# Kernel tuning notes

Hardware: AMD Instinct MI355X
Metric: run time of the kernel (lower is better)

Reference implementation:

```python
import jax, jax.numpy as jnp
import numpy as np

IN_DIM = 768
D_MODEL = 256
B, T = 64, 2048
LN_EPS = 1e-5


def setup_inputs() -> dict:
    key = jax.random.key(0)
    ks = jax.random.split(key, 8)
    s_in = 1.0 / np.sqrt(IN_DIM)
    s_d = 1.0 / np.sqrt(D_MODEL)
    return {
        "x": jax.random.normal(ks[0], (B, T, IN_DIM), dtype=jnp.float32),
        "ln_gamma": jnp.ones((IN_DIM,), jnp.float32),
        "ln_beta": jnp.zeros((IN_DIM,), jnp.float32),
        "W_proj": jax.random.uniform(ks[1], (IN_DIM, D_MODEL), jnp.float32, -s_in, s_in),
        "b_proj": jax.random.uniform(ks[2], (D_MODEL,), jnp.float32, -s_in, s_in),
        "W1": jax.random.uniform(ks[3], (D_MODEL, D_MODEL), jnp.float32, -s_d, s_d),
        "b1": jax.random.uniform(ks[4], (D_MODEL,), jnp.float32, -s_d, s_d),
        "W2": jax.random.uniform(ks[5], (D_MODEL,), jnp.float32, -s_d, s_d),
        "b2": jax.random.uniform(ks[6], (), jnp.float32, -s_d, s_d),
    }


def reference(x, ln_gamma, ln_beta, W_proj, b_proj, W1, b1, W2, b2):
    # nan/inf sanitization to 0
    x = jnp.nan_to_num(x, nan=0.0, posinf=0.0, neginf=0.0)
    # LayerNorm over last dim (biased variance, eps=1e-5)
    mu = jnp.mean(x, axis=-1, keepdims=True)
    var = jnp.mean(jnp.square(x - mu), axis=-1, keepdims=True)
    xn = (x - mu) * jax.lax.rsqrt(var + LN_EPS) * ln_gamma + ln_beta
    # projection to d_model: [B, T, D]
    h = jnp.einsum('btf,fd->btd', xn, W_proj) + b_proj
    # tanh-MLP attention scores: [B, T]
    a = jnp.tanh(jnp.einsum('btd,de->bte', h, W1) + b1)
    w = jnp.einsum('bte,e->bt', a, W2) + b2
    w = jax.nn.softmax(w, axis=-1)
    # weighted-sum pooling over T: [B, D]
    return jnp.einsum('btd,bt->bd', h, w)
```

## Files before the change

kernel.cpp:

```cpp
#include <hip/hip_runtime.h>

#define LN_EPS 1e-5f

typedef __attribute__((ext_vector_type(8))) short s8vec;
typedef __attribute__((ext_vector_type(4))) float f4vec;

#define OFF_WPT   0u
#define OFF_W1F   393216u
#define OFF_U     524288u
#define OFF_C     525312u
#define OFF_UPART 526336u
#define OFF_VPART 575488u
#define OFF_PM    624640u
#define OFF_PS    632832u
#define OFF_PO    641024u

#define BAR()     asm volatile("s_barrier" ::: "memory")
#define WAIT_V4() asm volatile("s_waitcnt vmcnt(4) lgkmcnt(0)" ::: "memory")
#define WAIT_V0() asm volatile("s_waitcnt vmcnt(0) lgkmcnt(0)" ::: "memory")
#define WAIT_L0() asm volatile("s_waitcnt lgkmcnt(0)" ::: "memory")
#define ORDER_FENCE() do { asm volatile("" ::: "memory"); \
                           __builtin_amdgcn_sched_barrier(0); } while (0)

__device__ __forceinline__ unsigned short f2bf(float f) {
  unsigned int u = __float_as_uint(f);
  u += 0x7fffu + ((u >> 16) & 1u);
  return (unsigned short)(u >> 16);
}
__device__ __forceinline__ float bf2f(unsigned short h) {
  return __uint_as_float(((unsigned int)h) << 16);
}
__device__ __forceinline__ void gll16(const void* g, void* l) {
  __builtin_amdgcn_global_load_lds(
      (const __attribute__((address_space(1))) unsigned int*)g,
      (__attribute__((address_space(3))) unsigned int*)l, 16, 0, 0);
}

__global__ void k0_prep(const float* __restrict__ Wp,
                        const float* __restrict__ gamma,
                        const float* __restrict__ beta,
                        const float* __restrict__ W1,
                        char* __restrict__ ws) {
  const int blk = blockIdx.x;
  const int n = threadIdx.x;
  if (blk < 48) {
    unsigned short* wpt = (unsigned short*)(ws + OFF_WPT);
    const int sw = (n & 7) << 4;
    const int k0 = blk * 16;
    float up = 0.f, vp = 0.f;
#pragma unroll
    for (int j = 0; j < 16; ++j) {
      const int k = k0 + j;
      const float w = Wp[k * 256 + n];
      const float wpv = gamma[k] * w;
      up += wpv;
      vp += beta[k] * w;
      const int c = k >> 6, kc = k & 63;
      wpt[c * 16384 + n * 64 + ((((kc * 2) ^ sw)) >> 1)] = f2bf(wpv);
    }
    ((float*)(ws + OFF_UPART))[blk * 256 + n] = up;
    ((float*)(ws + OFF_VPART))[blk * 256 + n] = vp;
  } else {
    unsigned short* w1f = (unsigned short*)(ws + OFF_W1F);
    const int d0 = (blk - 48) * 16;
    const int t = n >> 4, lre = n & 15;
#pragma unroll
    for (int jj = 0; jj < 16; ++jj) {
      const int d = d0 + jj;
      const int ks = d >> 5, lqd = (d >> 3) & 3, j = d & 7;
      w1f[(((t * 8 + ks) * 64) + lqd * 16 + lre) * 8 + j] = f2bf(W1[d * 256 + n]);
    }
  }
}

__global__ void k0_reduce(const float* __restrict__ bproj, char* __restrict__ ws) {
  const int n = threadIdx.x;
  const float* upart = (const float*)(ws + OFF_UPART);
  const float* vpart = (const float*)(ws + OFF_VPART);
  float u = 0.f, v = 0.f;
  for (int i = 0; i < 48; ++i) {
    u += upart[i * 256 + n];
    v += vpart[i * 256 + n];
  }
  ((float*)(ws + OFF_U))[n] = u;
  ((float*)(ws + OFF_C))[n] = v + bproj[n];
}

__global__ __launch_bounds__(256, 2)
void k1_main(const float* __restrict__ x,
             const float* __restrict__ b1,
             const float* __restrict__ W2,
             char* __restrict__ ws) {
  __shared__ __align__(16) char sm[40960];
  char* const sm_a = sm;
  char* const sm_b = sm + 8192;
  char* const sm_h = sm + 8192;
  float* const f_b1 = (float*)sm;
  float* const f_w2 = (float*)(sm + 1024);
  float* const f_lp = (float*)(sm + 2048);
  float* const f_lg = (float*)(sm + 3072);
  float* const f_e  = (float*)(sm + 3328);
  float* const f_mu = (float*)(sm + 3584);
  float* const f_iv = (float*)(sm + 3840);

  const int tid  = threadIdx.x;
  const int lane = tid & 63;
  const int wid  = tid >> 6;
  const int lr = lane & 15;
  const int lq = lane >> 4;

  const int arow = tid >> 2;
  const int aq   = tid & 3;
  const float* xrow = x + (size_t)(blockIdx.x * 64 + arow) * 768 + aq * 16;

  const char* bsrc = (const char*)ws + OFF_WPT + wid * 8192 + lane * 16;
  char*       bdst = sm_b + wid * 8192 + lane * 16;

  const f4vec fz = {0.f, 0.f, 0.f, 0.f};
  f4vec acc[4][4];
#pragma unroll
  for (int m = 0; m < 4; ++m)
#pragma unroll
    for (int n = 0; n < 4; ++n) acc[m][n] = fz;

  float s1 = 0.f, s2 = 0.f;
  float4 vaA[4], vaB[4];
#pragma unroll
  for (int j = 0; j < 4; ++j) vaA[j] = *(const float4*)(xrow + 0 * 64 + j * 4);
#pragma unroll
  for (int j = 0; j < 4; ++j) vaB[j] = *(const float4*)(xrow + 1 * 64 + j * 4);

  auto p1body = [&](int c, float4 (&va)[4], bool pf) {
#pragma unroll
    for (int s = 0; s < 8; ++s) gll16(bsrc + c * 32768 + s * 1024, bdst + s * 1024);
    ORDER_FENCE();
    float v[16];
#pragma unroll
    for (int j = 0; j < 4; ++j) {
      v[4*j+0] = va[j].x; v[4*j+1] = va[j].y; v[4*j+2] = va[j].z; v[4*j+3] = va[j].w;
    }
    unsigned int pk[8];
#pragma unroll
    for (int j = 0; j < 16; ++j) {
      float f = v[j];
      if ((__float_as_uint(f) & 0x7f800000u) == 0x7f800000u) f = 0.f;
      s1 += f; s2 += f * f;
      const unsigned int hb = f2bf(f);
      if ((j & 1) == 0) pk[j >> 1] = hb; else pk[j >> 1] |= hb << 16;
    }
    {
      const int base = arow * 128 + aq * 32;
      const int sw = (arow & 7) << 4;
      *(int4*)(sm_a + ((base     ) ^ sw)) = make_int4((int)pk[0], (int)pk[1], (int)pk[2], (int)pk[3]);
      *(int4*)(sm_a + ((base + 16) ^ sw)) = make_int4((int)pk[4], (int)pk[5], (int)pk[6], (int)pk[7]);
    }
    if (pf) {
#pragma unroll
      for (int j = 0; j < 4; ++j) va[j] = *(const float4*)(xrow + (c + 2) * 64 + j * 4);
    }
    if (pf) WAIT_V4(); else WAIT_V0();
    BAR();
#pragma unroll
    for (int ks = 0; ks < 2; ++ks) {
      const int kb = (ks * 32 + lq * 8) * 2;
      s8vec af[4], bfv[4];
#pragma unroll
      for (int m = 0; m < 4; ++m) {
        const int row = m * 16 + lr;
        af[m] = *(const s8vec*)(sm_a + ((row * 128 + kb) ^ ((row & 7) << 4)));
      }
#pragma unroll
      for (int n = 0; n < 4; ++n) {
        const int row = wid * 64 + n * 16 + lr;
        bfv[n] = *(const s8vec*)(sm_b + ((row * 128 + kb) ^ ((row & 7) << 4)));
      }
#pragma unroll
      for (int m = 0; m < 4; ++m)
#pragma unroll
        for (int n = 0; n < 4; ++n)
          acc[m][n] = __builtin_amdgcn_mfma_f32_16x16x32_bf16(af[m], bfv[n], acc[m][n], 0, 0, 0);
    }
    BAR();
  };

  for (int cc = 0; cc < 12; cc += 2) {
    p1body(cc,     vaA, cc + 2 < 12);
    p1body(cc + 1, vaB, cc + 3 < 12);
  }

  s1 += __shfl_xor(s1, 1); s1 += __shfl_xor(s1, 2);
  s2 += __shfl_xor(s2, 1); s2 += __shfl_xor(s2, 2);
  if (aq == 0) {
    const float mu = s1 * (1.f / 768.f);
    float var = s2 * (1.f / 768.f) - mu * mu;
    var = fmaxf(var, 0.f);
    f_mu[arow] = mu;
    f_iv[arow] = rsqrtf(var + LN_EPS);
  }
  f_b1[tid] = b1[tid];
  f_w2[tid] = W2[tid];
  float u4[4], c4[4];
#pragma unroll
  for (int n = 0; n < 4; ++n) {
    u4[n] = ((const float*)(ws + OFF_U))[wid * 64 + n * 16 + lr];
    c4[n] = ((const float*)(ws + OFF_C))[wid * 64 + n * 16 + lr];
  }
  WAIT_L0();
  BAR();

#pragma unroll
  for (int m = 0; m < 4; ++m) {
#pragma unroll
    for (int i = 0; i < 4; ++i) {
      const int rl = m * 16 + lq * 4 + i;
      const float mu  = f_mu[rl];
      const float inv = f_iv[rl];
      const int sw = (rl & 7) << 4;
#pragma unroll
      for (int n = 0; n < 4; ++n) {
        const int cd = wid * 64 + n * 16 + lr;
        const float h = inv * (acc[m][n][i] - mu * u4[n]) + c4[n];
        *(unsigned short*)(sm_h + ((rl * 512 + cd * 2) ^ sw)) = f2bf(h);
      }
    }
  }
  WAIT_L0();
  BAR();

  const char* w1f = (const char*)ws + OFF_W1F;
  f4vec acc2[4][4];
#pragma unroll
  for (int m = 0; m < 4; ++m)
#pragma unroll
    for (int n = 0; n < 4; ++n) acc2[m][n] = fz;

#pragma unroll
  for (int ks = 0; ks < 8; ++ks) {
    s8vec af[4], bf[4];
#pragma unroll
    for (int et = 0; et < 4; ++et)
      af[et] = *(const s8vec*)(w1f + (((wid * 4 + et) * 8 + ks) * 64 + lane) * 16);
#pragma unroll
    for (int rt = 0; rt < 4; ++rt) {
      const int r = rt * 16 + lr;
      bf[rt] = *(const s8vec*)(sm_h + ((r * 512 + ks * 64 + lq * 16) ^ ((r & 7) << 4)));
    }
#pragma unroll
    for (int et = 0; et < 4; ++et)
#pragma unroll
      for (int rt = 0; rt < 4; ++rt)
        acc2[et][rt] = __builtin_amdgcn_mfma_f32_16x16x32_bf16(af[et], bf[rt], acc2[et][rt], 0, 0, 0);
  }

  float lp[4] = {0.f, 0.f, 0.f, 0.f};
#pragma unroll
  for (int et = 0; et < 4; ++et) {
#pragma unroll
    for (int i = 0; i < 4; ++i) {
      const int e = wid * 64 + et * 16 + lq * 4 + i;
      const float b1v = f_b1[e];
      const float w2v = f_w2[e];
#pragma unroll
      for (int rt = 0; rt < 4; ++rt) {
        float z = acc2[et][rt][i] + b1v;
        z = fminf(fmaxf(z, -15.f), 15.f);
        const float e2 = __expf(2.f * z);
        const float a = (e2 - 1.f) / (e2 + 1.f);
        lp[rt] += a * w2v;
      }
    }
  }
#pragma unroll
  for (int rt = 0; rt < 4; ++rt) {
    float t = lp[rt];
    t += __shfl_xor(t, 16);
    t += __shfl_xor(t, 32);
    if (lq == 0) f_lp[(rt * 16 + lr) * 4 + wid] = t;
  }
  __syncthreads();
  if (tid < 64)
    f_lg[tid] = f_lp[tid*4+0] + f_lp[tid*4+1] + f_lp[tid*4+2] + f_lp[tid*4+3];
  __syncthreads();

  float mx = -1e30f;
  for (int r = 0; r < 64; ++r) mx = fmaxf(mx, f_lg[r]);
  if (tid < 64) f_e[tid] = __expf(f_lg[tid] - mx);
  __syncthreads();

  {
    const int d = tid;
    float o = 0.f;
    for (int r = 0; r < 64; ++r) {
      const float ev = f_e[r];
      const unsigned short hb =
          *(const unsigned short*)(sm_h + ((r * 512 + d * 2) ^ ((r & 7) << 4)));
      o += ev * bf2f(hb);
    }
    ((float*)(ws + OFF_PO))[blockIdx.x * 256 + d] = o;
  }
  if (tid == 0) {
    float s = 0.f;
    for (int r = 0; r < 64; ++r) s += f_e[r];
    ((float*)(ws + OFF_PS))[blockIdx.x] = s;
    ((float*)(ws + OFF_PM))[blockIdx.x] = mx;
  }
}

__global__ void k2_combine(const char* __restrict__ ws, float* __restrict__ out) {
  const int b = blockIdx.x;
  const int d = threadIdx.x;
  const float* pm = (const float*)(ws + OFF_PM) + b * 32;
  const float* ps = (const float*)(ws + OFF_PS) + b * 32;
  const float* po = (const float*)(ws + OFF_PO) + (size_t)b * 32 * 256;
  float mx = -1e30f;
  for (int c = 0; c < 32; ++c) mx = fmaxf(mx, pm[c]);
  float num = 0.f, den = 0.f;
  for (int c = 0; c < 32; ++c) {
    const float al = __expf(pm[c] - mx);
    den += al * ps[c];
    num += al * po[c * 256 + d];
  }
  out[b * 256 + d] = num / den;
}

extern "C" void kernel_launch(void* const* d_in, const int* in_sizes, int n_in,
                              void* d_out, int out_size, void* d_ws, size_t ws_size,
                              hipStream_t stream) {
  const float* x     = (const float*)d_in[0];
  const float* gamma = (const float*)d_in[1];
  const float* beta  = (const float*)d_in[2];
  const float* Wp    = (const float*)d_in[3];
  const float* bproj = (const float*)d_in[4];
  const float* W1    = (const float*)d_in[5];
  const float* b1    = (const float*)d_in[6];
  const float* W2    = (const float*)d_in[7];
  char* ws = (char*)d_ws;
  float* out = (float*)d_out;

  k0_prep   <<<dim3(64),   dim3(256), 0, stream>>>(Wp, gamma, beta, W1, ws);
  k0_reduce <<<dim3(1),    dim3(256), 0, stream>>>(bproj, ws);
  k1_main   <<<dim3(2048), dim3(256), 0, stream>>>(x, b1, W2, ws);
  k2_combine<<<dim3(64),   dim3(256), 0, stream>>>(ws, out);
}
```

Measured before the change: 154.5 us.

## Load projection weights directly into registers in MFMA fragment layout; double-buffer A tile

The prep kernel now writes the gamma-scaled projection weights pre-arranged in MFMA B-fragment order, so the main kernel loads B fragments straight from global memory into registers instead of staging them through LDS with global_load_lds. The A tile (bf16-converted x) is double-buffered in LDS, so packing the next chunk overlaps with the MFMAs of the current one, and each chunk needs only one barrier. This cuts LDS traffic and shrinks shared memory. In exchange, weight fragments are fetched per wave from L2 with no LDS reuse, and the hand-written vmcnt waits are dropped, leaving scheduling to the compiler.

```diff
diff --git a/kernel.cpp b/kernel.cpp
--- a/kernel.cpp
+++ b/kernel.cpp
@@ -5,7 +5,7 @@
 typedef __attribute__((ext_vector_type(8))) short s8vec;
 typedef __attribute__((ext_vector_type(4))) float f4vec;
 
-#define OFF_WPT   0u
+#define OFF_WPF   0u
 #define OFF_W1F   393216u
 #define OFF_U     524288u
 #define OFF_C     525312u
@@ -16,11 +16,7 @@
 #define OFF_PO    641024u
 
 #define BAR()     asm volatile("s_barrier" ::: "memory")
-#define WAIT_V4() asm volatile("s_waitcnt vmcnt(4) lgkmcnt(0)" ::: "memory")
-#define WAIT_V0() asm volatile("s_waitcnt vmcnt(0) lgkmcnt(0)" ::: "memory")
 #define WAIT_L0() asm volatile("s_waitcnt lgkmcnt(0)" ::: "memory")
-#define ORDER_FENCE() do { asm volatile("" ::: "memory"); \
-                           __builtin_amdgcn_sched_barrier(0); } while (0)
 
 __device__ __forceinline__ unsigned short f2bf(float f) {
   unsigned int u = __float_as_uint(f);
@@ -29,11 +25,6 @@
 }
 __device__ __forceinline__ float bf2f(unsigned short h) {
   return __uint_as_float(((unsigned int)h) << 16);
-}
-__device__ __forceinline__ void gll16(const void* g, void* l) {
-  __builtin_amdgcn_global_load_lds(
-      (const __attribute__((address_space(1))) unsigned int*)g,
-      (__attribute__((address_space(3))) unsigned int*)l, 16, 0, 0);
 }
 
 __global__ void k0_prep(const float* __restrict__ Wp,
@@ -44,8 +35,8 @@
   const int blk = blockIdx.x;
   const int n = threadIdx.x;
   if (blk < 48) {
-    unsigned short* wpt = (unsigned short*)(ws + OFF_WPT);
-    const int sw = (n & 7) << 4;
+    unsigned short* wpf = (unsigned short*)(ws + OFF_WPF);
+    const int wid = n >> 6, nn = (n >> 4) & 3, lr = n & 15;
     const int k0 = blk * 16;
     float up = 0.f, vp = 0.f;
 #pragma unroll
@@ -55,8 +46,8 @@
       const float wpv = gamma[k] * w;
       up += wpv;
       vp += beta[k] * w;
-      const int c = k >> 6, kc = k & 63;
-      wpt[c * 16384 + n * 64 + ((((kc * 2) ^ sw)) >> 1)] = f2bf(wpv);
+      const int c = k >> 6, ks = (k >> 5) & 1, lqd = (k >> 3) & 3, jj = k & 7;
+      wpf[(((((c * 4 + wid) * 2 + ks) * 4 + nn) * 64) + lqd * 16 + lr) * 8 + jj] = f2bf(wpv);
     }
     ((float*)(ws + OFF_UPART))[blk * 256 + n] = up;
     ((float*)(ws + OFF_VPART))[blk * 256 + n] = vp;
@@ -91,17 +82,15 @@
              const float* __restrict__ b1,
              const float* __restrict__ W2,
              char* __restrict__ ws) {
-  __shared__ __align__(16) char sm[40960];
-  char* const sm_a = sm;
-  char* const sm_b = sm + 8192;
-  char* const sm_h = sm + 8192;
-  float* const f_b1 = (float*)sm;
-  float* const f_w2 = (float*)(sm + 1024);
-  float* const f_lp = (float*)(sm + 2048);
-  float* const f_lg = (float*)(sm + 3072);
-  float* const f_e  = (float*)(sm + 3328);
-  float* const f_mu = (float*)(sm + 3584);
-  float* const f_iv = (float*)(sm + 3840);
+  __shared__ __align__(16) char sm[36864];
+  char* const sm_h = sm;
+  float* const f_b1 = (float*)(sm + 32768);
+  float* const f_w2 = (float*)(sm + 33792);
+  float* const f_lp = (float*)(sm + 34816);
+  float* const f_lg = (float*)(sm + 35840);
+  float* const f_e  = (float*)(sm + 36096);
+  float* const f_mu = (float*)(sm + 36352);
+  float* const f_iv = (float*)(sm + 36608);
 
   const int tid  = threadIdx.x;
   const int lane = tid & 63;
@@ -113,8 +102,7 @@
   const int aq   = tid & 3;
   const float* xrow = x + (size_t)(blockIdx.x * 64 + arow) * 768 + aq * 16;
 
-  const char* bsrc = (const char*)ws + OFF_WPT + wid * 8192 + lane * 16;
-  char*       bdst = sm_b + wid * 8192 + lane * 16;
+  const char* wpf = (const char*)ws + OFF_WPF + wid * 8192 + lane * 16;
 
   const f4vec fz = {0.f, 0.f, 0.f, 0.f};
   f4vec acc[4][4];
@@ -124,68 +112,64 @@
     for (int n = 0; n < 4; ++n) acc[m][n] = fz;
 
   float s1 = 0.f, s2 = 0.f;
-  float4 vaA[4], vaB[4];
-#pragma unroll
-  for (int j = 0; j < 4; ++j) vaA[j] = *(const float4*)(xrow + 0 * 64 + j * 4);
-#pragma unroll
-  for (int j = 0; j < 4; ++j) vaB[j] = *(const float4*)(xrow + 1 * 64 + j * 4);
-
-  auto p1body = [&](int c, float4 (&va)[4], bool pf) {
-#pragma unroll
-    for (int s = 0; s < 8; ++s) gll16(bsrc + c * 32768 + s * 1024, bdst + s * 1024);
-    ORDER_FENCE();
-    float v[16];
+  float xv[16];
+
+  auto loadx = [&](int c) {
 #pragma unroll
     for (int j = 0; j < 4; ++j) {
-      v[4*j+0] = va[j].x; v[4*j+1] = va[j].y; v[4*j+2] = va[j].z; v[4*j+3] = va[j].w;
-    }
+      const float4 t = *(const float4*)(xrow + c * 64 + j * 4);
+      xv[4*j+0] = t.x; xv[4*j+1] = t.y; xv[4*j+2] = t.z; xv[4*j+3] = t.w;
+    }
+  };
+  auto packA = [&](int p) {
     unsigned int pk[8];
 #pragma unroll
     for (int j = 0; j < 16; ++j) {
-      float f = v[j];
+      float f = xv[j];
       if ((__float_as_uint(f) & 0x7f800000u) == 0x7f800000u) f = 0.f;
       s1 += f; s2 += f * f;
       const unsigned int hb = f2bf(f);
       if ((j & 1) == 0) pk[j >> 1] = hb; else pk[j >> 1] |= hb << 16;
     }
-    {
-      const int base = arow * 128 + aq * 32;
-      const int sw = (arow & 7) << 4;
-      *(int4*)(sm_a + ((base     ) ^ sw)) = make_int4((int)pk[0], (int)pk[1], (int)pk[2], (int)pk[3]);
-      *(int4*)(sm_a + ((base + 16) ^ sw)) = make_int4((int)pk[4], (int)pk[5], (int)pk[6], (int)pk[7]);
-    }
-    if (pf) {
-#pragma unroll
-      for (int j = 0; j < 4; ++j) va[j] = *(const float4*)(xrow + (c + 2) * 64 + j * 4);
-    }
-    if (pf) WAIT_V4(); else WAIT_V0();
-    BAR();
+    const int base = arow * 128 + aq * 32;
+    const int sw = (arow & 7) << 4;
+    char* ab = sm + p * 8192;
+    *(int4*)(ab + ((base     ) ^ sw)) = make_int4((int)pk[0], (int)pk[1], (int)pk[2], (int)pk[3]);
+    *(int4*)(ab + ((base + 16) ^ sw)) = make_int4((int)pk[4], (int)pk[5], (int)pk[6], (int)pk[7]);
+  };
+
+  loadx(0);
+  packA(0);
+  loadx(1);
+  WAIT_L0(); BAR();
+
+  for (int c = 0; c < 12; ++c) {
+    s8vec bfv[8];
+#pragma unroll
+    for (int ks = 0; ks < 2; ++ks)
+#pragma unroll
+      for (int n = 0; n < 4; ++n)
+        bfv[ks * 4 + n] =
+            *(const s8vec*)(wpf + (size_t)(((c * 4) * 2 + ks) * 4 + n) * 1024);
+    if (c < 11) packA((c + 1) & 1);
+    if (c < 10) loadx(c + 2);
 #pragma unroll
     for (int ks = 0; ks < 2; ++ks) {
       const int kb = (ks * 32 + lq * 8) * 2;
-      s8vec af[4], bfv[4];
+      s8vec af[4];
 #pragma unroll
       for (int m = 0; m < 4; ++m) {
         const int row = m * 16 + lr;
-        af[m] = *(const s8vec*)(sm_a + ((row * 128 + kb) ^ ((row & 7) << 4)));
+        af[m] = *(const s8vec*)(sm + (c & 1) * 8192 + ((row * 128 + kb) ^ ((row & 7) << 4)));
       }
 #pragma unroll
-      for (int n = 0; n < 4; ++n) {
-        const int row = wid * 64 + n * 16 + lr;
-        bfv[n] = *(const s8vec*)(sm_b + ((row * 128 + kb) ^ ((row & 7) << 4)));
-      }
-#pragma unroll
       for (int m = 0; m < 4; ++m)
 #pragma unroll
         for (int n = 0; n < 4; ++n)
-          acc[m][n] = __builtin_amdgcn_mfma_f32_16x16x32_bf16(af[m], bfv[n], acc[m][n], 0, 0, 0);
-    }
+          acc[m][n] = __builtin_amdgcn_mfma_f32_16x16x32_bf16(af[m], bfv[ks * 4 + n], acc[m][n], 0, 0, 0);
+    }
+    WAIT_L0();
     BAR();
-  };
-
-  for (int cc = 0; cc < 12; cc += 2) {
-    p1body(cc,     vaA, cc + 2 < 12);
-    p1body(cc + 1, vaB, cc + 3 < 12);
   }
 
   s1 += __shfl_xor(s1, 1); s1 += __shfl_xor(s1, 2);
```

After: 160.6 us. 1.04x slower.

## Split main kernel work across 512-thread blocks with eight waves per tile

Applied to the files above, without the earlier changes.

Doubles the main kernel's block size to 512 threads. Each of the eight waves now owns half as many output columns in both GEMMs, and each thread loads and converts eight input floats instead of sixteen. The weighted-sum pooling is split into two halves over rows, producing twice as many partial outputs that the combine kernel adds together. The goal is more resident waves to hide global-load latency on the memory-bound input stream. In exchange, the tighter launch bounds may force register spills, the workspace partial-output region doubles in size, and there is more barrier traffic per block.

```diff
diff --git a/kernel.cpp b/kernel.cpp
--- a/kernel.cpp
+++ b/kernel.cpp
@@ -16,7 +16,7 @@
 #define OFF_PO    641024u
 
 #define BAR()     asm volatile("s_barrier" ::: "memory")
-#define WAIT_V4() asm volatile("s_waitcnt vmcnt(4) lgkmcnt(0)" ::: "memory")
+#define WAIT_V2() asm volatile("s_waitcnt vmcnt(2) lgkmcnt(0)" ::: "memory")
 #define WAIT_V0() asm volatile("s_waitcnt vmcnt(0) lgkmcnt(0)" ::: "memory")
 #define WAIT_L0() asm volatile("s_waitcnt lgkmcnt(0)" ::: "memory")
 #define ORDER_FENCE() do { asm volatile("" ::: "memory"); \
@@ -86,7 +86,7 @@
   ((float*)(ws + OFF_C))[n] = v + bproj[n];
 }
 
-__global__ __launch_bounds__(256, 2)
+__global__ __launch_bounds__(512, 4)
 void k1_main(const float* __restrict__ x,
              const float* __restrict__ b1,
              const float* __restrict__ W2,
@@ -98,10 +98,10 @@
   float* const f_b1 = (float*)sm;
   float* const f_w2 = (float*)(sm + 1024);
   float* const f_lp = (float*)(sm + 2048);
-  float* const f_lg = (float*)(sm + 3072);
-  float* const f_e  = (float*)(sm + 3328);
-  float* const f_mu = (float*)(sm + 3584);
-  float* const f_iv = (float*)(sm + 3840);
+  float* const f_lg = (float*)(sm + 4096);
+  float* const f_e  = (float*)(sm + 4352);
+  float* const f_mu = (float*)(sm + 4608);
+  float* const f_iv = (float*)(sm + 4864);
 
   const int tid  = threadIdx.x;
   const int lane = tid & 63;
@@ -109,75 +109,67 @@
   const int lr = lane & 15;
   const int lq = lane >> 4;
 
-  const int arow = tid >> 2;
-  const int aq   = tid & 3;
-  const float* xrow = x + (size_t)(blockIdx.x * 64 + arow) * 768 + aq * 16;
-
-  const char* bsrc = (const char*)ws + OFF_WPT + wid * 8192 + lane * 16;
-  char*       bdst = sm_b + wid * 8192 + lane * 16;
+  const int arow = tid >> 3;
+  const int aq   = tid & 7;
+  const float* xrow = x + (size_t)(blockIdx.x * 64 + arow) * 768 + aq * 8;
+
+  const char* bsrc = (const char*)ws + OFF_WPT + wid * 4096 + lane * 16;
+  char*       bdst = sm_b + wid * 4096 + lane * 16;
 
   const f4vec fz = {0.f, 0.f, 0.f, 0.f};
-  f4vec acc[4][4];
+  f4vec acc[4][2];
 #pragma unroll
   for (int m = 0; m < 4; ++m)
 #pragma unroll
-    for (int n = 0; n < 4; ++n) acc[m][n] = fz;
+    for (int n = 0; n < 2; ++n) acc[m][n] = fz;
 
   float s1 = 0.f, s2 = 0.f;
-  float4 vaA[4], vaB[4];
-#pragma unroll
-  for (int j = 0; j < 4; ++j) vaA[j] = *(const float4*)(xrow + 0 * 64 + j * 4);
-#pragma unroll
-  for (int j = 0; j < 4; ++j) vaB[j] = *(const float4*)(xrow + 1 * 64 + j * 4);
-
-  auto p1body = [&](int c, float4 (&va)[4], bool pf) {
-#pragma unroll
-    for (int s = 0; s < 8; ++s) gll16(bsrc + c * 32768 + s * 1024, bdst + s * 1024);
+  float4 vaA[2], vaB[2];
+  vaA[0] = *(const float4*)(xrow +  0); vaA[1] = *(const float4*)(xrow +  4);
+  vaB[0] = *(const float4*)(xrow + 64); vaB[1] = *(const float4*)(xrow + 68);
+
+  auto p1body = [&](int c, float4 (&va)[2], bool pf) {
+#pragma unroll
+    for (int s = 0; s < 4; ++s) gll16(bsrc + c * 32768 + s * 1024, bdst + s * 1024);
     ORDER_FENCE();
-    float v[16];
-#pragma unroll
-    for (int j = 0; j < 4; ++j) {
-      v[4*j+0] = va[j].x; v[4*j+1] = va[j].y; v[4*j+2] = va[j].z; v[4*j+3] = va[j].w;
-    }
-    unsigned int pk[8];
-#pragma unroll
-    for (int j = 0; j < 16; ++j) {
+    float v[8];
+    v[0]=va[0].x; v[1]=va[0].y; v[2]=va[0].z; v[3]=va[0].w;
+    v[4]=va[1].x; v[5]=va[1].y; v[6]=va[1].z; v[7]=va[1].w;
+    unsigned int pk[4];
+#pragma unroll
+    for (int j = 0; j < 8; ++j) {
       float f = v[j];
       if ((__float_as_uint(f) & 0x7f800000u) == 0x7f800000u) f = 0.f;
       s1 += f; s2 += f * f;
       const unsigned int hb = f2bf(f);
       if ((j & 1) == 0) pk[j >> 1] = hb; else pk[j >> 1] |= hb << 16;
     }
-    {
-      const int base = arow * 128 + aq * 32;
-      const int sw = (arow & 7) << 4;
-      *(int4*)(sm_a + ((base     ) ^ sw)) = make_int4((int)pk[0], (int)pk[1], (int)pk[2], (int)pk[3]);
-      *(int4*)(sm_a + ((base + 16) ^ sw)) = make_int4((int)pk[4], (int)pk[5], (int)pk[6], (int)pk[7]);
-    }
+    *(int4*)(sm_a + ((arow * 128 + aq * 16) ^ ((arow & 7) << 4))) =
+        make_int4((int)pk[0], (int)pk[1], (int)pk[2], (int)pk[3]);
     if (pf) {
-#pragma unroll
-      for (int j = 0; j < 4; ++j) va[j] = *(const float4*)(xrow + (c + 2) * 64 + j * 4);
-    }
-    if (pf) WAIT_V4(); else WAIT_V0();
+      va[0] = *(const float4*)(xrow + (c + 2) * 64);
+      va[1] = *(const float4*)(xrow + (c + 2) * 64 + 4);
+    }
+    if (pf) WAIT_V2(); else WAIT_V0();
     BAR();
 #pragma unroll
     for (int ks = 0; ks < 2; ++ks) {
       const int kb = (ks * 32 + lq * 8) * 2;
-      s8vec af[4], bfv[4];
+      s8vec af[4], bfv[2];
 #pragma unroll
       for (int m = 0; m < 4; ++m) {
         const int row = m * 16 + lr;
         af[m] = *(const s8vec*)(sm_a + ((row * 128 + kb) ^ ((row & 7) << 4)));
       }
 #pragma unroll
-      for (int n = 0; n < 4; ++n) {
-        const int row = wid * 64 + n * 16 + lr;
-        bfv[n] = *(const s8vec*)(sm_b + ((row * 128 + kb) ^ ((row & 7) << 4)));
+      for (int n = 0; n < 2; ++n) {
+        const int bcol = wid * 32 + n * 16 + lr;
+        bfv[n] = *(const s8vec*)(sm_b + ((bcol * 128 + kb) ^ ((bcol & 7) << 4)));
       }
 #pragma unroll
       for (int m = 0; m < 4; ++m)
 #pragma unroll
-        for (int n = 0; n < 4; ++n)
+        for (int n = 0; n < 2; ++n)
           acc[m][n] = __builtin_amdgcn_mfma_f32_16x16x32_bf16(af[m], bfv[n], acc[m][n], 0, 0, 0);
     }
     BAR();
@@ -188,8 +180,8 @@
     p1body(cc + 1, vaB, cc + 3 < 12);
   }
 
-  s1 += __shfl_xor(s1, 1); s1 += __shfl_xor(s1, 2);
-  s2 += __shfl_xor(s2, 1); s2 += __shfl_xor(s2, 2);
+  s1 += __shfl_xor(s1, 1); s1 += __shfl_xor(s1, 2); s1 += __shfl_xor(s1, 4);
+  s2 += __shfl_xor(s2, 1); s2 += __shfl_xor(s2, 2); s2 += __shfl_xor(s2, 4);
   if (aq == 0) {
     const float mu = s1 * (1.f / 768.f);
     float var = s2 * (1.f / 768.f) - mu * mu;
@@ -197,13 +189,15 @@
     f_mu[arow] = mu;
     f_iv[arow] = rsqrtf(var + LN_EPS);
   }
-  f_b1[tid] = b1[tid];
-  f_w2[tid] = W2[tid];
-  float u4[4], c4[4];
-#pragma unroll
-  for (int n = 0; n < 4; ++n) {
-    u4[n] = ((const float*)(ws + OFF_U))[wid * 64 + n * 16 + lr];
-    c4[n] = ((const float*)(ws + OFF_C))[wid * 64 + n * 16 + lr];
+  if (tid < 256) {
+    f_b1[tid] = b1[tid];
+    f_w2[tid] = W2[tid];
+  }
+  float u2[2], c2[2];
+#pragma unroll
+  for (int n = 0; n < 2; ++n) {
+    u2[n] = ((const float*)(ws + OFF_U))[wid * 32 + n * 16 + lr];
+    c2[n] = ((const float*)(ws + OFF_C))[wid * 32 + n * 16 + lr];
   }
   WAIT_L0();
   BAR();
@@ -217,9 +211,9 @@
       const float inv = f_iv[rl];
       const int sw = (rl & 7) << 4;
 #pragma unroll
-      for (int n = 0; n < 4; ++n) {
-        const int cd = wid * 64 + n * 16 + lr;
-        const float h = inv * (acc[m][n][i] - mu * u4[n]) + c4[n];
+      for (int n = 0; n < 2; ++n) {
+        const int cd = wid * 32 + n * 16 + lr;
+        const float h = inv * (acc[m][n][i] - mu * u2[n]) + c2[n];
         *(unsigned short*)(sm_h + ((rl * 512 + cd * 2) ^ sw)) = f2bf(h);
       }
     }
@@ -228,25 +222,25 @@
   BAR();
 
   const char* w1f = (const char*)ws + OFF_W1F;
-  f4vec acc2[4][4];
-#pragma unroll
-  for (int m = 0; m < 4; ++m)
+  f4vec acc2[2][4];
+#pragma unroll
+  for (int m = 0; m < 2; ++m)
 #pragma unroll
     for (int n = 0; n < 4; ++n) acc2[m][n] = fz;
 
 #pragma unroll
   for (int ks = 0; ks < 8; ++ks) {
-    s8vec af[4], bf[4];
-#pragma unroll
-    for (int et = 0; et < 4; ++et)
-      af[et] = *(const s8vec*)(w1f + (((wid * 4 + et) * 8 + ks) * 64 + lane) * 16);
+    s8vec af[2], bf[4];
+#pragma unroll
+    for (int et = 0; et < 2; ++et)
+      af[et] = *(const s8vec*)(w1f + (((wid * 2 + et) * 8 + ks) * 64 + lane) * 16);
 #pragma unroll
     for (int rt = 0; rt < 4; ++rt) {
       const int r = rt * 16 + lr;
       bf[rt] = *(const s8vec*)(sm_h + ((r * 512 + ks * 64 + lq * 16) ^ ((r & 7) << 4)));
     }
 #pragma unroll
-    for (int et = 0; et < 4; ++et)
+    for (int et = 0; et < 2; ++et)
 #pragma unroll
       for (int rt = 0; rt < 4; ++rt)
         acc2[et][rt] = __builtin_amdgcn_mfma_f32_16x16x32_bf16(af[et], bf[rt], acc2[et][rt], 0, 0, 0);
@@ -254,10 +248,10 @@
 
   float lp[4] = {0.f, 0.f, 0.f, 0.f};
 #pragma unroll
-  for (int et = 0; et < 4; ++et) {
+  for (int et = 0; et < 2; ++et) {
 #pragma unroll
     for (int i = 0; i < 4; ++i) {
-      const int e = wid * 64 + et * 16 + lq * 4 + i;
+      const int e = (wid * 2 + et) * 16 + lq * 4 + i;
       const float b1v = f_b1[e];
       const float w2v = f_w2[e];
 #pragma unroll
@@ -275,11 +269,15 @@
     float t = lp[rt];
     t += __shfl_xor(t, 16);
     t += __shfl_xor(t, 32);
-    if (lq == 0) f_lp[(rt * 16 + lr) * 4 + wid] = t;
+    if (lq == 0) f_lp[(rt * 16 + lr) * 8 + wid] = t;
   }
   __syncthreads();
-  if (tid < 64)
-    f_lg[tid] = f_lp[tid*4+0] + f_lp[tid*4+1] + f_lp[tid*4+2] + f_lp[tid*4+3];
+  if (tid < 64) {
+    float s = 0.f;
+#pragma unroll
+    for (int w = 0; w < 8; ++w) s += f_lp[tid * 8 + w];
+    f_lg[tid] = s;
+  }
   __syncthreads();
 
   float mx = -1e30f;
@@ -288,15 +286,16 @@
   __syncthreads();
 
   {
-    const int d = tid;
+    const int d = tid & 255;
+    const int half = tid >> 8;
     float o = 0.f;
-    for (int r = 0; r < 64; ++r) {
+    for (int r = half * 32; r < half * 32 + 32; ++r) {
       const float ev = f_e[r];
       const unsigned short hb =
           *(const unsigned short*)(sm_h + ((r * 512 + d * 2) ^ ((r & 7) << 4)));
       o += ev * bf2f(hb);
     }
-    ((float*)(ws + OFF_PO))[blockIdx.x * 256 + d] = o;
+    ((float*)(ws + OFF_PO))[blockIdx.x * 512 + half * 256 + d] = o;
   }
   if (tid == 0) {
     float s = 0.f;
@@ -311,14 +310,14 @@
   const int d = threadIdx.x;
   const float* pm = (const float*)(ws + OFF_PM) + b * 32;
   const float* ps = (const float*)(ws + OFF_PS) + b * 32;
-  const float* po = (const float*)(ws + OFF_PO) + (size_t)b * 32 * 256;
+  const float* po = (const float*)(ws + OFF_PO) + (size_t)b * 32 * 512;
   float mx = -1e30f;
   for (int c = 0; c < 32; ++c) mx = fmaxf(mx, pm[c]);
   float num = 0.f, den = 0.f;
   for (int c = 0; c < 32; ++c) {
     const float al = __expf(pm[c] - mx);
     den += al * ps[c];
-    num += al * po[c * 256 + d];
+    num += al * (po[c * 512 + d] + po[c * 512 + 256 + d]);
   }
   out[b * 256 + d] = num / den;
 }
@@ -339,6 +338,6 @@
 
   k0_prep   <<<dim3(64),   dim3(256), 0, stream>>>(Wp, gamma, beta, W1, ws);
   k0_reduce <<<dim3(1),    dim3(256), 0, stream>>>(bproj, ws);
-  k1_main   <<<dim3(2048), dim3(256), 0, stream>>>(x, b1, W2, ws);
+  k1_main   <<<dim3(2048), dim3(512), 0, stream>>>(x, b1, W2, ws);
   k2_combine<<<dim3(64),   dim3(256), 0, stream>>>(ws, out);
 }
```

Result: slower. 157.7 us (+2.0%).
